# Kernel optimization log

Hardware: AMD Instinct MI355X
Metric: run time of the kernel (lower is better)

Reference implementation:

```python
import jax, jax.numpy as jnp
import numpy as np

B, N, D, F, NDRV, PASSES = 64, 50000, 16, 5, 1000, 4


def setup_inputs() -> dict:
    key = jax.random.key(0)
    ks = jax.random.split(key, 12)
    inp = {
        "x": jax.random.normal(ks[0], (B, N), jnp.float32),
        "neighbor_idx": jax.random.randint(ks[1], (N, D), 0, N),
        "driver_idx": jnp.sort(jax.random.randint(ks[2], (NDRV,), 0, N)),
    }
    # conv stack: 1->5, five of 5->5, 5->1 (kernel [1,3])
    chans = [(1, F)] + [(F, F)] * 5 + [(F, 1)]
    for i, (ci, co) in enumerate(chans):
        inp[f"w{i}"] = jax.random.normal(ks[3 + i], (co, ci, 1, 3), jnp.float32) * 0.1
        inp[f"b{i}"] = jnp.zeros((co,), jnp.float32)
    return inp


def _conv1x3(z, w, b):
    # z: [B,C,N,W], w: [O,C,1,3] -> [B,O,N,W-2]
    out = jax.lax.conv_general_dilated(
        z, w, window_strides=(1, 1), padding='VALID',
        dimension_numbers=('NCHW', 'OIHW', 'NCHW'))
    return out + b[None, :, None, None]


def reference(x, neighbor_idx, driver_idx,
              w0, b0, w1, b1, w2, b2, w3, b3, w4, b4, w5, b5, w6, b6):
    params = [(w0, b0), (w1, b1), (w2, b2), (w3, b3), (w4, b4), (w5, b5), (w6, b6)]
    z = x  # [B, N]
    for _ in range(PASSES):
        g = z[:, neighbor_idx]            # neighbor gather -> [B, N, D]
        h = g[:, None]                    # [B, 1, N, D]  (input_preprocessor output)
        for w, b in params:
            h = jax.nn.relu(_conv1x3(h, w, b))  # relu after every conv (all but pool)
        h = 0.5 * (h[..., :-1] + h[..., 1:])    # AvgPool [1,2] stride 1: width 2 -> 1
        z = h.reshape(x.shape[0], -1)           # [B, N] (single channel, width 1)
    # final: mean over singleton channel dim then driver gather == direct gather
    return z[:, driver_idx]                      # [B, NDRV]
```

## Files before the change

### kernel.cpp

```cpp
#include <hip/hip_runtime.h>

#define NB    50000
#define BB    64
#define DD    16
#define NDRVN 1000

typedef float f2 __attribute__((ext_vector_type(2)));

__device__ __forceinline__ float vg(float s) {
    asm("" : "+v"(s));
    return s;
}

__device__ __forceinline__ f2 pf(f2 a, f2 b, f2 c) {
    return __builtin_elementwise_fma(a, b, c);
}
__device__ __forceinline__ f2 relu2(f2 a) {
    return __builtin_elementwise_max(a, (f2)0.0f);
}
__device__ __forceinline__ f2 splat(float s) {
    float v = vg(s);
    return (f2){v, v};
}

__global__ __launch_bounds__(256) void transpose_kernel(
    const float* __restrict__ x, float* __restrict__ xT)
{
    int tid = blockIdx.x * 256 + threadIdx.x;
    int n = tid >> 6;
    int b = tid & 63;
    if (n < NB) xT[tid] = x[b * NB + n];
}

template<int WIN>
__device__ __forceinline__ void conv5p(const f2 (&in)[5][14], f2 (&out)[5][14],
                                       const float* __restrict__ w,
                                       const float* __restrict__ bias)
{
    constexpr int WOUT = WIN - 2;
    f2 wr[75];
#pragma unroll
    for (int t = 0; t < 75; ++t) wr[t] = splat(w[t]);
    f2 bb[5];
#pragma unroll
    for (int c = 0; c < 5; ++c) bb[c] = splat(bias[c]);

#pragma unroll
    for (int x = 0; x < WOUT; ++x) {
#pragma unroll
        for (int c = 0; c < 5; ++c) {
            f2 acc = bb[c];
#pragma unroll
            for (int ci = 0; ci < 5; ++ci) {
                acc = pf(wr[c * 15 + ci * 3 + 0], in[ci][x + 0], acc);
                acc = pf(wr[c * 15 + ci * 3 + 1], in[ci][x + 1], acc);
                acc = pf(wr[c * 15 + ci * 3 + 2], in[ci][x + 2], acc);
            }
            out[c][x] = relu2(acc);
        }
    }
}

__global__ __launch_bounds__(256)
__attribute__((amdgpu_waves_per_eu(2, 8)))
void pass_kernel(
    const float* __restrict__ zin, float* __restrict__ zout,
    const int*  __restrict__ nidx,
    const float* __restrict__ w0, const float* __restrict__ b0,
    const float* __restrict__ w1, const float* __restrict__ b1,
    const float* __restrict__ w2, const float* __restrict__ b2,
    const float* __restrict__ w3, const float* __restrict__ b3,
    const float* __restrict__ w4, const float* __restrict__ b4,
    const float* __restrict__ w5, const float* __restrict__ b5,
    const float* __restrict__ w6, const float* __restrict__ b6)
{
    int lane   = threadIdx.x & 63;
    int waveid = blockIdx.x * 4 + (threadIdx.x >> 6);
    int n0 = __builtin_amdgcn_readfirstlane(waveid * 2);

    const int* ip = nidx + n0 * DD;

    f2 g[16];
#pragma unroll
    for (int d = 0; d < 16; ++d) {
        float a = zin[(size_t)ip[d]      * BB + lane];
        float b = zin[(size_t)ip[16 + d] * BB + lane];
        g[d] = (f2){a, b};
    }

    f2 ha[5][14], hb[5][14];

    {
        f2 wr[15], bb[5];
#pragma unroll
        for (int t = 0; t < 15; ++t) wr[t] = splat(w0[t]);
#pragma unroll
        for (int c = 0; c < 5; ++c) bb[c] = splat(b0[c]);
#pragma unroll
        for (int x = 0; x < 14; ++x) {
#pragma unroll
            for (int c = 0; c < 5; ++c) {
                f2 acc = bb[c];
                acc = pf(wr[c * 3 + 0], g[x + 0], acc);
                acc = pf(wr[c * 3 + 1], g[x + 1], acc);
                acc = pf(wr[c * 3 + 2], g[x + 2], acc);
                ha[c][x] = relu2(acc);
            }
        }
    }

    conv5p<14>(ha, hb, w1, b1);
    conv5p<12>(hb, ha, w2, b2);
    conv5p<10>(ha, hb, w3, b3);
    conv5p<8> (hb, ha, w4, b4);
    conv5p<6> (ha, hb, w5, b5);

    {
        f2 wr[15];
#pragma unroll
        for (int t = 0; t < 15; ++t) wr[t] = splat(w6[t]);
        f2 bias = splat(b6[0]);
        f2 t0 = bias, t1 = bias;
#pragma unroll
        for (int ci = 0; ci < 5; ++ci) {
            t0 = pf(wr[ci * 3 + 0], hb[ci][0], t0);
            t0 = pf(wr[ci * 3 + 1], hb[ci][1], t0);
            t0 = pf(wr[ci * 3 + 2], hb[ci][2], t0);
            t1 = pf(wr[ci * 3 + 0], hb[ci][1], t1);
            t1 = pf(wr[ci * 3 + 1], hb[ci][2], t1);
            t1 = pf(wr[ci * 3 + 2], hb[ci][3], t1);
        }
        t0 = relu2(t0);
        t1 = relu2(t1);
        f2 o;
        o.x = 0.5f * (t0.x + t1.x);
        o.y = 0.5f * (t0.y + t1.y);
        zout[(size_t)n0 * BB + lane]       = o.x;
        zout[(size_t)(n0 + 1) * BB + lane] = o.y;
    }
}

__global__ __launch_bounds__(256) void gather_out_kernel(
    const float* __restrict__ z, const int* __restrict__ didx,
    float* __restrict__ out)
{
    int i = blockIdx.x * 256 + threadIdx.x;
    if (i >= BB * NDRVN) return;
    int b = i / NDRVN;
    int k = i - b * NDRVN;
    out[i] = z[(size_t)didx[k] * BB + b];
}

extern "C" void kernel_launch(void* const* d_in, const int* in_sizes, int n_in,
                              void* d_out, int out_size, void* d_ws, size_t ws_size,
                              hipStream_t stream)
{
    const float* x    = (const float*)d_in[0];
    const int*   nidx = (const int*)  d_in[1];
    const int*   didx = (const int*)  d_in[2];
    const float* w[7];
    const float* b[7];
    for (int i = 0; i < 7; ++i) {
        w[i] = (const float*)d_in[3 + 2 * i];
        b[i] = (const float*)d_in[4 + 2 * i];
    }

    float* z0 = (float*)d_ws;
    float* z1 = z0 + (size_t)NB * BB;

    const int tblocks = (NB * BB) / 256;
    const int pblocks = NB / 8;

    transpose_kernel<<<tblocks, 256, 0, stream>>>(x, z0);

    pass_kernel<<<pblocks, 256, 0, stream>>>(z0, z1, nidx,
        w[0], b[0], w[1], b[1], w[2], b[2], w[3], b[3],
        w[4], b[4], w[5], b[5], w[6], b[6]);
    pass_kernel<<<pblocks, 256, 0, stream>>>(z1, z0, nidx,
        w[0], b[0], w[1], b[1], w[2], b[2], w[3], b[3],
        w[4], b[4], w[5], b[5], w[6], b[6]);
    pass_kernel<<<pblocks, 256, 0, stream>>>(z0, z1, nidx,
        w[0], b[0], w[1], b[1], w[2], b[2], w[3], b[3],
        w[4], b[4], w[5], b[5], w[6], b[6]);
    pass_kernel<<<pblocks, 256, 0, stream>>>(z1, z0, nidx,
        w[0], b[0], w[1], b[1], w[2], b[2], w[3], b[3],
        w[4], b[4], w[5], b[5], w[6], b[6]);

    gather_out_kernel<<<(BB * NDRVN + 255) / 256, 256, 0, stream>>>(z0, didx, (float*)d_out);
}
```

Measured before the change: 921.1 us.

## Replace packed-FP32 two-node-per-wave conv with scalar one-node-per-wave

Drops the packed float2 (v_pk_fma) path, where each wave processed two nodes, and moves to scalar fmaf with one node per wave. The grid doubles and waves_per_eu is pinned to 2. The aim is to halve register pressure and raise parallelism for the gather. In exchange it gives up packed FMA throughput, and it may limit occupancy through the fixed waves-per-EU hint.

```diff
diff --git a/kernel.cpp b/kernel.cpp
--- a/kernel.cpp
+++ b/kernel.cpp
@@ -5,22 +5,9 @@
 #define DD    16
 #define NDRVN 1000
 
-typedef float f2 __attribute__((ext_vector_type(2)));
-
 __device__ __forceinline__ float vg(float s) {
     asm("" : "+v"(s));
     return s;
-}
-
-__device__ __forceinline__ f2 pf(f2 a, f2 b, f2 c) {
-    return __builtin_elementwise_fma(a, b, c);
-}
-__device__ __forceinline__ f2 relu2(f2 a) {
-    return __builtin_elementwise_max(a, (f2)0.0f);
-}
-__device__ __forceinline__ f2 splat(float s) {
-    float v = vg(s);
-    return (f2){v, v};
 }
 
 __global__ __launch_bounds__(256) void transpose_kernel(
@@ -33,36 +20,38 @@
 }
 
 template<int WIN>
-__device__ __forceinline__ void conv5p(const f2 (&in)[5][14], f2 (&out)[5][14],
-                                       const float* __restrict__ w,
-                                       const float* __restrict__ bias)
+__device__ __forceinline__ void conv5(const float (&in)[5][14], float (&out)[5][14],
+                                      const float* __restrict__ w,
+                                      const float* __restrict__ b)
 {
     constexpr int WOUT = WIN - 2;
-    f2 wr[75];
+    float wr[75];
 #pragma unroll
-    for (int t = 0; t < 75; ++t) wr[t] = splat(w[t]);
-    f2 bb[5];
+    for (int t = 0; t < 75; ++t) wr[t] = vg(w[t]);
+    float bb[5];
 #pragma unroll
-    for (int c = 0; c < 5; ++c) bb[c] = splat(bias[c]);
+    for (int c = 0; c < 5; ++c) bb[c] = vg(b[c]);
 
 #pragma unroll
     for (int x = 0; x < WOUT; ++x) {
 #pragma unroll
         for (int c = 0; c < 5; ++c) {
-            f2 acc = bb[c];
+            float acc = fmaf(wr[c * 15 + 0], in[0][x + 0], bb[c]);
+            acc = fmaf(wr[c * 15 + 1], in[0][x + 1], acc);
+            acc = fmaf(wr[c * 15 + 2], in[0][x + 2], acc);
 #pragma unroll
-            for (int ci = 0; ci < 5; ++ci) {
-                acc = pf(wr[c * 15 + ci * 3 + 0], in[ci][x + 0], acc);
-                acc = pf(wr[c * 15 + ci * 3 + 1], in[ci][x + 1], acc);
-                acc = pf(wr[c * 15 + ci * 3 + 2], in[ci][x + 2], acc);
+            for (int ci = 1; ci < 5; ++ci) {
+                acc = fmaf(wr[c * 15 + ci * 3 + 0], in[ci][x + 0], acc);
+                acc = fmaf(wr[c * 15 + ci * 3 + 1], in[ci][x + 1], acc);
+                acc = fmaf(wr[c * 15 + ci * 3 + 2], in[ci][x + 2], acc);
             }
-            out[c][x] = relu2(acc);
+            out[c][x] = fmaxf(acc, 0.0f);
         }
     }
 }
 
 __global__ __launch_bounds__(256)
-__attribute__((amdgpu_waves_per_eu(2, 8)))
+__attribute__((amdgpu_waves_per_eu(2, 2)))
 void pass_kernel(
     const float* __restrict__ zin, float* __restrict__ zout,
     const int*  __restrict__ nidx,
@@ -74,69 +63,66 @@
     const float* __restrict__ w5, const float* __restrict__ b5,
     const float* __restrict__ w6, const float* __restrict__ b6)
 {
-    int lane   = threadIdx.x & 63;
-    int waveid = blockIdx.x * 4 + (threadIdx.x >> 6);
-    int n0 = __builtin_amdgcn_readfirstlane(waveid * 2);
+    int lane = threadIdx.x & 63;
+    int wv   = blockIdx.x * 4 + (threadIdx.x >> 6);
+    int n    = __builtin_amdgcn_readfirstlane(wv);
 
-    const int* ip = nidx + n0 * DD;
+    const int* ip = nidx + n * DD;
 
-    f2 g[16];
+    float g[16];
 #pragma unroll
-    for (int d = 0; d < 16; ++d) {
-        float a = zin[(size_t)ip[d]      * BB + lane];
-        float b = zin[(size_t)ip[16 + d] * BB + lane];
-        g[d] = (f2){a, b};
-    }
+    for (int d = 0; d < 16; ++d)
+        g[d] = zin[(size_t)ip[d] * BB + lane];
 
-    f2 ha[5][14], hb[5][14];
+    float ha[5][14], hb[5][14];
 
     {
-        f2 wr[15], bb[5];
+        float wr[15], bb[5];
 #pragma unroll
-        for (int t = 0; t < 15; ++t) wr[t] = splat(w0[t]);
+        for (int t = 0; t < 15; ++t) wr[t] = vg(w0[t]);
 #pragma unroll
-        for (int c = 0; c < 5; ++c) bb[c] = splat(b0[c]);
+        for (int c = 0; c < 5; ++c) bb[c] = vg(b0[c]);
 #pragma unroll
         for (int x = 0; x < 14; ++x) {
 #pragma unroll
             for (int c = 0; c < 5; ++c) {
-                f2 acc = bb[c];
-                acc = pf(wr[c * 3 + 0], g[x + 0], acc);
-                acc = pf(wr[c * 3 + 1], g[x + 1], acc);
-                acc = pf(wr[c * 3 + 2], g[x + 2], acc);
-                ha[c][x] = relu2(acc);
+                float acc = fmaf(wr[c * 3 + 0], g[x + 0], bb[c]);
+                acc = fmaf(wr[c * 3 + 1], g[x + 1], acc);
+                acc = fmaf(wr[c * 3 + 2], g[x + 2], acc);
+                ha[c][x] = fmaxf(acc, 0.0f);
             }
         }
     }
 
-    conv5p<14>(ha, hb, w1, b1);
-    conv5p<12>(hb, ha, w2, b2);
-    conv5p<10>(ha, hb, w3, b3);
-    conv5p<8> (hb, ha, w4, b4);
-    conv5p<6> (ha, hb, w5, b5);
+    conv5<14>(ha, hb, w1, b1);
+    conv5<12>(hb, ha, w2, b2);
+    conv5<10>(ha, hb, w3, b3);
+    conv5<8> (hb, ha, w4, b4);
+    conv5<6> (ha, hb, w5, b5);
 
     {
-        f2 wr[15];
+        float wr[15];
 #pragma unroll
-        for (int t = 0; t < 15; ++t) wr[t] = splat(w6[t]);
-        f2 bias = splat(b6[0]);
-        f2 t0 = bias, t1 = bias;
+        for (int t = 0; t < 15; ++t) wr[t] = vg(w6[t]);
+        float bias = vg(b6[0]);
+
+        float t0 = fmaf(wr[0], hb[0][0], bias);
+        float t1 = fmaf(wr[0], hb[0][1], bias);
+        t0 = fmaf(wr[1], hb[0][1], t0);
+        t0 = fmaf(wr[2], hb[0][2], t0);
+        t1 = fmaf(wr[1], hb[0][2], t1);
+        t1 = fmaf(wr[2], hb[0][3], t1);
 #pragma unroll
-        for (int ci = 0; ci < 5; ++ci) {
-            t0 = pf(wr[ci * 3 + 0], hb[ci][0], t0);
-            t0 = pf(wr[ci * 3 + 1], hb[ci][1], t0);
-            t0 = pf(wr[ci * 3 + 2], hb[ci][2], t0);
-            t1 = pf(wr[ci * 3 + 0], hb[ci][1], t1);
-            t1 = pf(wr[ci * 3 + 1], hb[ci][2], t1);
-            t1 = pf(wr[ci * 3 + 2], hb[ci][3], t1);
+        for (int ci = 1; ci < 5; ++ci) {
+#pragma unroll
+            for (int t = 0; t < 3; ++t) {
+                t0 = fmaf(wr[ci * 3 + t], hb[ci][0 + t], t0);
+                t1 = fmaf(wr[ci * 3 + t], hb[ci][1 + t], t1);
+            }
         }
-        t0 = relu2(t0);
-        t1 = relu2(t1);
-        f2 o;
-        o.x = 0.5f * (t0.x + t1.x);
-        o.y = 0.5f * (t0.y + t1.y);
-        zout[(size_t)n0 * BB + lane]       = o.x;
-        zout[(size_t)(n0 + 1) * BB + lane] = o.y;
+        t0 = fmaxf(t0, 0.0f);
+        t1 = fmaxf(t1, 0.0f);
+        zout[(size_t)n * BB + lane] = 0.5f * (t0 + t1);
     }
 }
 
@@ -169,7 +155,7 @@
     float* z1 = z0 + (size_t)NB * BB;
 
     const int tblocks = (NB * BB) / 256;
-    const int pblocks = NB / 8;
+    const int pblocks = NB / 4;
 
     transpose_kernel<<<tblocks, 256, 0, stream>>>(x, z0);
 
```

New measurement: 1.036 ms. 1.12x slower.
